# Performance work log

Measured on AMD Instinct MI355X. Metric: run time of the kernel, lower is better.

The kernel has to match this reference:

```python
import jax, jax.numpy as jnp
import numpy as np

N = 50000          # total nodes (types: 20000/17000/13000)
E = 800000         # edges, avg degree 16
NUM_ETYPES = 6
ALPHA = 0.05       # residual-attention blend coefficient
SLOPE = 0.2        # leaky_relu negative slope


def _edge_softmax(e, dst, n):
    # softmax over incoming edges of each destination node; e: [E, H]
    m = jax.ops.segment_max(e, dst, num_segments=n)      # [N, H]
    ex = jnp.exp(e - m[dst])
    s = jax.ops.segment_sum(ex, dst, num_segments=n)     # [N, H]
    return ex / s[dst]


def _gat_layer(h, src, dst, etype, W, We, eemb, al, ar, ae, resW, res_attn, activate):
    n = h.shape[0]
    H, out = al.shape
    feat = (h @ W).reshape(n, H, out)                    # [N, H, out]
    T, edim = eemb.shape
    # edge-type attention term: embedding -> fc_e -> attn_e; only T distinct rows
    et_att = jnp.einsum('thd,hd->th', (eemb @ We).reshape(T, H, edim), ae)  # [T, H]
    el = jnp.einsum('nho,ho->nh', feat, al)              # [N, H]
    er = jnp.einsum('nho,ho->nh', feat, ar)              # [N, H]
    e = jax.nn.leaky_relu(el[src] + er[dst] + et_att[etype], SLOPE)  # [E, H]
    a = _edge_softmax(e, dst, n)                         # [E, H]
    if res_attn is not None:
        a = a * (1.0 - ALPHA) + res_attn * ALPHA
    rst = jax.ops.segment_sum(feat[src] * a[:, :, None], dst, num_segments=n)  # [N, H, out]
    if resW is not None:
        rst = rst + (h @ resW).reshape(n, H, out)
    if activate:
        rst = jax.nn.elu(rst)
    return rst, jax.lax.stop_gradient(a)


def _forward(x0, x1, x2, fcw0, fcb0, fcw1, fcb1, fcw2, fcb2,
             W0, We0, eemb0, al0, ar0, ae0,
             W1, We1, eemb1, al1, ar1, ae1, resW1,
             W2, We2, eemb2, al2, ar2, ae2, resW2,
             src, dst, etype):
    # per-type input projection then concat (feat_drop=0 -> identity)
    h = jnp.concatenate([x0 @ fcw0 + fcb0, x1 @ fcw1 + fcb1, x2 @ fcw2 + fcb2], axis=0)  # [N, 64]
    h1, a = _gat_layer(h, src, dst, etype, W0, We0, eemb0, al0, ar0, ae0, None, None, True)
    h1 = h1.reshape(h1.shape[0], -1)                     # [N, 256]
    h2, a = _gat_layer(h1, src, dst, etype, W1, We1, eemb1, al1, ar1, ae1, resW1, a, True)
    h2 = h2.reshape(h2.shape[0], -1)                     # [N, 256]
    logits, _ = _gat_layer(h2, src, dst, etype, W2, We2, eemb2, al2, ar2, ae2, resW2, None, False)
    return logits                                        # [N, 1, 16]


def setup_inputs():
    key = jax.random.key(0)
    ks = iter(jax.random.split(key, 48))
    def rn(shape, fan_in):
        return jax.random.normal(next(ks), shape, jnp.float32) / np.sqrt(fan_in)
    inp = {}
    inp['x0'] = jax.random.normal(next(ks), (20000, 128), jnp.float32)
    inp['x1'] = jax.random.normal(next(ks), (17000, 256), jnp.float32)
    inp['x2'] = jax.random.normal(next(ks), (13000, 64), jnp.float32)
    inp['fcw0'] = rn((128, 64), 128); inp['fcb0'] = jnp.zeros((64,), jnp.float32)
    inp['fcw1'] = rn((256, 64), 256); inp['fcb1'] = jnp.zeros((64,), jnp.float32)
    inp['fcw2'] = rn((64, 64), 64);   inp['fcb2'] = jnp.zeros((64,), jnp.float32)
    # layer 0: in=64 -> H=8, out=32
    inp['W0'] = rn((64, 256), 64); inp['We0'] = rn((64, 512), 64)
    inp['eemb0'] = rn((NUM_ETYPES, 64), 1.0)
    inp['al0'] = rn((8, 32), 32); inp['ar0'] = rn((8, 32), 32); inp['ae0'] = rn((8, 64), 64)
    # layer 1: in=256 -> H=8, out=32, residual
    inp['W1'] = rn((256, 256), 256); inp['We1'] = rn((64, 512), 64)
    inp['eemb1'] = rn((NUM_ETYPES, 64), 1.0)
    inp['al1'] = rn((8, 32), 32); inp['ar1'] = rn((8, 32), 32); inp['ae1'] = rn((8, 64), 64)
    inp['resW1'] = rn((256, 256), 256)
    # output layer: in=256 -> H=1, out=16, residual
    inp['W2'] = rn((256, 16), 256); inp['We2'] = rn((64, 64), 64)
    inp['eemb2'] = rn((NUM_ETYPES, 64), 1.0)
    inp['al2'] = rn((1, 16), 16); inp['ar2'] = rn((1, 16), 16); inp['ae2'] = rn((1, 64), 64)
    inp['resW2'] = rn((256, 16), 256)
    inp['src'] = jax.random.randint(next(ks), (E,), 0, N)
    inp['dst'] = jax.random.randint(next(ks), (E,), 0, N)
    inp['etype'] = jax.random.randint(next(ks), (E,), 0, NUM_ETYPES)
    return inp


def reference(x0, x1, x2, fcw0, fcb0, fcw1, fcb1, fcw2, fcb2,
              W0, We0, eemb0, al0, ar0, ae0,
              W1, We1, eemb1, al1, ar1, ae1, resW1,
              W2, We2, eemb2, al2, ar2, ae2, resW2,
              src, dst, etype):
    return _forward(x0, x1, x2, fcw0, fcb0, fcw1, fcb1, fcw2, fcb2,
                    W0, We0, eemb0, al0, ar0, ae0,
                    W1, We1, eemb1, al1, ar1, ae1, resW1,
                    W2, We2, eemb2, al2, ar2, ae2, resW2,
                    src, dst, etype)
```

## Files before the change

### kernel.cpp

```cpp
#include <hip/hip_runtime.h>
#include <hip/hip_bf16.h>

#define ALPHA 0.05f
#define SLOPE 0.2f
#define LCAP 128

typedef __attribute__((ext_vector_type(8))) short short8v;
typedef __attribute__((ext_vector_type(8))) unsigned short ushort8v;
typedef __attribute__((ext_vector_type(4))) float floatx4;

__device__ inline ushort f2b(float f) {
    uint u = __float_as_uint(f);
    return (ushort)((u + 0x7fffu + ((u >> 16) & 1u)) >> 16);
}
__device__ inline float b2f(ushort b) { return __uint_as_float(((uint)b) << 16); }

__device__ inline void gload_lds16(const ushort* g, ushort* l) {
    __builtin_amdgcn_global_load_lds(
        (const __attribute__((address_space(1))) uint*)g,
        (__attribute__((address_space(3))) uint*)l, 16, 0, 0);
}


__global__ void hist_kernel(const int* __restrict__ dst, int* __restrict__ counts, int E) {
    int e = blockIdx.x * blockDim.x + threadIdx.x;
    if (e < E) atomicAdd(&counts[dst[e]], 1);
}

__global__ __launch_bounds__(256) void scan_part(const int* __restrict__ counts,
                                                 int* __restrict__ offsets,
                                                 int* __restrict__ partial, int n) {
    __shared__ int sd[256];
    int i = blockIdx.x * 256 + threadIdx.x;
    int v = (i < n) ? counts[i] : 0;
    sd[threadIdx.x] = v;
    __syncthreads();
    for (int off = 1; off < 256; off <<= 1) {
        int t = (threadIdx.x >= off) ? sd[threadIdx.x - off] : 0;
        __syncthreads();
        sd[threadIdx.x] += t;
        __syncthreads();
    }
    if (i < n) offsets[i + 1] = sd[threadIdx.x];
    if (threadIdx.x == 255) partial[blockIdx.x] = sd[255];
}

__global__ __launch_bounds__(256) void scan_top(int* __restrict__ partial, int nb) {
    __shared__ int sd[256];
    int v = (threadIdx.x < nb) ? partial[threadIdx.x] : 0;
    sd[threadIdx.x] = v;
    __syncthreads();
    for (int off = 1; off < 256; off <<= 1) {
        int t = (threadIdx.x >= off) ? sd[threadIdx.x - off] : 0;
        __syncthreads();
        sd[threadIdx.x] += t;
        __syncthreads();
    }
    if (threadIdx.x < nb) partial[threadIdx.x] = sd[threadIdx.x];
}

__global__ __launch_bounds__(256) void scan_add(int* __restrict__ offsets,
                                                int* __restrict__ cursor,
                                                const int* __restrict__ partial, int n) {
    int i = blockIdx.x * 256 + threadIdx.x;
    if (i >= n) return;
    int add = (blockIdx.x > 0) ? partial[blockIdx.x - 1] : 0;
    int v = offsets[i + 1] + add;
    offsets[i + 1] = v;
    if (i + 1 < n) cursor[i + 1] = v;
    if (i == 0) { offsets[0] = 0; cursor[0] = 0; }
}

__global__ void scatter_kernel(const int* __restrict__ src, const int* __restrict__ dst,
                               const int* __restrict__ et, int* __restrict__ cursor,
                               int* __restrict__ se, int E) {
    int e = blockIdx.x * blockDim.x + threadIdx.x;
    if (e >= E) return;
    int d = dst[e];
    int pos = atomicAdd(&cursor[d], 1);
    se[pos] = (src[e] << 3) | et[e];
}


__global__ void wprep3(const float* __restrict__ W0f, const float* __restrict__ W1f,
                       const float* __restrict__ WRf, ushort* __restrict__ Wt0,
                       ushort* __restrict__ Wt1, ushort* __restrict__ WtR) {
    int i = blockIdx.x * blockDim.x + threadIdx.x;
    if (i < 16384) {
        int k = i / 256, n = i % 256;
        Wt0[n * 64 + k] = f2b(W0f[i]);
    } else if (i < 16384 + 65536) {
        int j = i - 16384;
        int k = j / 256, n = j % 256;
        Wt1[n * 256 + k] = f2b(W1f[j]);
    } else if (i < 16384 + 2 * 65536) {
        int j = i - 16384 - 65536;
        int k = j / 256, n = j % 256;
        WtR[n * 256 + k] = f2b(WRf[j]);
    }
}


template<bool ATTN>
__global__ __launch_bounds__(256) void gemm_bf16(const ushort* __restrict__ A,
                                                 const ushort* __restrict__ Bt,
                                                 ushort* __restrict__ Cb,
                                                 const float* __restrict__ al,
                                                 const float* __restrict__ ar,
                                                 float* __restrict__ el,
                                                 float* __restrict__ er,
                                                 int M, int N, int K) {
    __shared__ ushort As[128 * 32];
    __shared__ ushort Bs[128 * 32];
    int bm = blockIdx.y * 128, bn = blockIdx.x * 128;
    int tid = threadIdx.x;
    int wave = tid >> 6, lane = tid & 63;
    int wm = (wave >> 1) * 64, wn = (wave & 1) * 64;
    int r = tid >> 2, c = (tid & 3) * 8;
    floatx4 acc[4][4] = {};
    for (int k0 = 0; k0 < K; k0 += 32) {
        gload_lds16(&A[(long)(bm + r) * K + k0 + c],       &As[(size_t)tid * 8]);
        gload_lds16(&A[(long)(bm + 64 + r) * K + k0 + c],  &As[(size_t)(256 + tid) * 8]);
        gload_lds16(&Bt[(long)(bn + r) * K + k0 + c],      &Bs[(size_t)tid * 8]);
        gload_lds16(&Bt[(long)(bn + 64 + r) * K + k0 + c], &Bs[(size_t)(256 + tid) * 8]);
        __syncthreads();
        int lr = lane & 15, lk = (lane >> 4) * 8;
        short8v af[4], bfr[4];
#pragma unroll
        for (int i = 0; i < 4; ++i)
            af[i] = *reinterpret_cast<const short8v*>(&As[(wm + i * 16 + lr) * 32 + lk]);
#pragma unroll
        for (int j = 0; j < 4; ++j)
            bfr[j] = *reinterpret_cast<const short8v*>(&Bs[(wn + j * 16 + lr) * 32 + lk]);
#pragma unroll
        for (int i = 0; i < 4; ++i)
#pragma unroll
            for (int j = 0; j < 4; ++j)
                acc[i][j] = __builtin_amdgcn_mfma_f32_16x16x32_bf16(af[i], bfr[j], acc[i][j], 0, 0, 0);
        __syncthreads();
    }
    int col = lane & 15, rbase = (lane >> 4) * 4;
#pragma unroll
    for (int i = 0; i < 4; ++i) {
#pragma unroll
        for (int rr = 0; rr < 4; ++rr) {
            int gm = bm + wm + i * 16 + rbase + rr;
            if (gm >= M) continue;
#pragma unroll
            for (int j = 0; j < 4; ++j) {
                int gn = bn + wn + j * 16 + col;
                Cb[(long)gm * N + gn] = f2b(acc[i][j][rr]);
            }
        }
    }
    if (ATTN) {
        int hA = (bn + wn) >> 5;
        float alv[4], arv[4];
#pragma unroll
        for (int j = 0; j < 4; ++j) {
            int h = hA + (j >> 1);
            int o = (j & 1) * 16 + col;
            alv[j] = al[h * 32 + o];
            arv[j] = ar[h * 32 + o];
        }
#pragma unroll
        for (int i = 0; i < 4; ++i) {
#pragma unroll
            for (int rr = 0; rr < 4; ++rr) {
                float slA = acc[i][0][rr] * alv[0] + acc[i][1][rr] * alv[1];
                float slB = acc[i][2][rr] * alv[2] + acc[i][3][rr] * alv[3];
                float srA = acc[i][0][rr] * arv[0] + acc[i][1][rr] * arv[1];
                float srB = acc[i][2][rr] * arv[2] + acc[i][3][rr] * arv[3];
#pragma unroll
                for (int off = 1; off < 16; off <<= 1) {
                    slA += __shfl_xor(slA, off, 64);
                    slB += __shfl_xor(slB, off, 64);
                    srA += __shfl_xor(srA, off, 64);
                    srB += __shfl_xor(srB, off, 64);
                }
                int gm = bm + wm + i * 16 + rbase + rr;
                if (col == 0 && gm < M) {
                    el[gm * 8 + hA]     = slA;
                    el[gm * 8 + hA + 1] = slB;
                    er[gm * 8 + hA]     = srA;
                    er[gm * 8 + hA + 1] = srB;
                }
            }
        }
    }
}


__global__ __launch_bounds__(256) void matmul64_fc3(
    const float* __restrict__ A0, const float* __restrict__ A1, const float* __restrict__ A2,
    const float* __restrict__ W0, const float* __restrict__ W1, const float* __restrict__ W2,
    const float* __restrict__ b0, const float* __restrict__ b1, const float* __restrict__ b2,
    ushort* __restrict__ C, int n0, int n1, int n2) {
    int z = blockIdx.z;
    const float *A, *W, *bias;
    int M, K;
    long coff;
    if (z == 0)      { A = A0; W = W0; bias = b0; M = n0; K = 128; coff = 0; }
    else if (z == 1) { A = A1; W = W1; bias = b1; M = n1; K = 256; coff = (long)n0 * 64; }
    else             { A = A2; W = W2; bias = b2; M = n2; K = 64;  coff = (long)(n0 + n1) * 64; }
    int bm = blockIdx.y * 64;
    if (bm >= M) return;
    __shared__ float As[16][68];
    __shared__ float Bs[16][68];
    int tx = threadIdx.x % 16, ty = threadIdx.x / 16;
    float acc[4][4] = {};
    for (int k0 = 0; k0 < K; k0 += 16) {
        for (int i = threadIdx.x; i < 64 * 16; i += 256) {
            int mm = i / 16, kk = i % 16;
            int gm = bm + mm;
            As[kk][mm] = (gm < M) ? A[(long)gm * K + k0 + kk] : 0.f;
        }
        for (int i = threadIdx.x; i < 16 * 64; i += 256) {
            int kk = i / 64, nn = i % 64;
            Bs[kk][nn] = W[(long)(k0 + kk) * 64 + nn];
        }
        __syncthreads();
#pragma unroll
        for (int kk = 0; kk < 16; ++kk) {
            float a[4], b[4];
#pragma unroll
            for (int i = 0; i < 4; ++i) a[i] = As[kk][ty * 4 + i];
#pragma unroll
            for (int j = 0; j < 4; ++j) b[j] = Bs[kk][tx * 4 + j];
#pragma unroll
            for (int i = 0; i < 4; ++i)
#pragma unroll
                for (int j = 0; j < 4; ++j) acc[i][j] += a[i] * b[j];
        }
        __syncthreads();
    }
#pragma unroll
    for (int i = 0; i < 4; ++i) {
        int gm = bm + ty * 4 + i;
        if (gm >= M) continue;
#pragma unroll
        for (int j = 0; j < 4; ++j) {
            int gn = tx * 4 + j;
            C[coff + (long)gm * 64 + gn] = f2b(acc[i][j] + bias[gn]);
        }
    }
}


template<bool ACC, bool BF16OUT, bool ATTN>
__global__ __launch_bounds__(256) void matmul_n16b(const ushort* __restrict__ A,
                                                   const float* __restrict__ W,
                                                   float* __restrict__ Cf,
                                                   ushort* __restrict__ Cb,
                                                   const float* __restrict__ al,
                                                   const float* __restrict__ ar,
                                                   float* __restrict__ el,
                                                   float* __restrict__ er, int M, int K) {
    __shared__ float Ws[256 * 16];
    for (int i = threadIdx.x; i < K * 16; i += 256) Ws[i] = W[i];
    __syncthreads();
    int m = blockIdx.x * 16 + threadIdx.x / 16;
    int nn = threadIdx.x % 16;
    if (m >= M) return;
    float s = 0.f;
    for (int k8 = 0; k8 < K / 8; ++k8) {
        uint4 v = *reinterpret_cast<const uint4*>(&A[(long)m * K + k8 * 8]);
        const uint* vp = reinterpret_cast<const uint*>(&v);
#pragma unroll
        for (int q = 0; q < 4; ++q) {
            uint w2 = vp[q];
            float f0 = __uint_as_float((w2 & 0xffffu) << 16);
            float f1 = __uint_as_float(w2 & 0xffff0000u);
            int k = k8 * 8 + q * 2;
            s += f0 * Ws[(k + 0) * 16 + nn] + f1 * Ws[(k + 1) * 16 + nn];
        }
    }
    if (BF16OUT) {
        Cb[(long)m * 16 + nn] = f2b(s);
    } else {
        if (ACC) s += Cf[(long)m * 16 + nn];
        Cf[(long)m * 16 + nn] = s;
    }
    if (ATTN) {
        float sl = s * al[nn], sr = s * ar[nn];
#pragma unroll
        for (int off = 1; off < 16; off <<= 1) {
            sl += __shfl_xor(sl, off, 64);
            sr += __shfl_xor(sr, off, 64);
        }
        if (nn == 0) { el[m] = sl; er[m] = sr; }
    }
}


template<int H>
__global__ __launch_bounds__(H * 64) void etype_att(const float* __restrict__ eemb,
                                                    const float* __restrict__ We,
                                                    const float* __restrict__ ae,
                                                    float* __restrict__ out) {
    __shared__ float es[64];
    int t = blockIdx.x;
    int j = threadIdx.x;
    if (j < 64) es[j] = eemb[t * 64 + j];
    __syncthreads();
    float wsum = 0.f;
#pragma unroll 8
    for (int k = 0; k < 64; ++k) wsum += es[k] * We[k * (H * 64) + j];
    float v = wsum * ae[j];
#pragma unroll
    for (int off = 32; off > 0; off >>= 1) v += __shfl_down(v, off, 64);
    if ((j & 63) == 0) out[t * H + (j >> 6)] = v;
}


template<bool BLEND, bool SAVE, bool RES>
__global__ __launch_bounds__(64) void fused_edge_h8(
    const int* __restrict__ offsets, const int* __restrict__ se,
    const float* __restrict__ el, const float* __restrict__ er,
    const float* __restrict__ etatt,
    const ushort* __restrict__ featb,
    const ushort* __restrict__ a0_in, ushort* __restrict__ a0_out,
    const ushort* __restrict__ resin, ushort* __restrict__ outb, int N) {
    int d = blockIdx.x;
    int lane = threadIdx.x;
    int lo = offsets[d], hi = offsets[d + 1];
    int deg = hi - lo;
    __shared__ float a_lds[LCAP][8];
    __shared__ int   s_lds[LCAP];
    __shared__ float er_s[8];
    __shared__ float m_s[8], inv_s[8];
    if (lane < 8) er_s[lane] = er[d * 8 + lane];
    __syncthreads();
    bool fast = (deg <= LCAP);
    if (fast) {
        for (int i = lane; i < deg * 8; i += 64) {
            int p = i >> 3, h = i & 7;
            int v0 = se[lo + p];
            int s = v0 >> 3, t = v0 & 7;
            if (h == 0) s_lds[p] = s;
            float v = el[s * 8 + h] + er_s[h] + etatt[t * 8 + h];
            a_lds[p][h] = v > 0.f ? v : SLOPE * v;
        }
        __syncthreads();
        {
            int g = lane >> 3, h = lane & 7;
            float m = -INFINITY;
            for (int p = g; p < deg; p += 8) m = fmaxf(m, a_lds[p][h]);
#pragma unroll
            for (int off = 8; off < 64; off <<= 1) m = fmaxf(m, __shfl_xor(m, off, 64));
            float ssum = 0.f;
            for (int p = g; p < deg; p += 8) ssum += __expf(a_lds[p][h] - m);
#pragma unroll
            for (int off = 8; off < 64; off <<= 1) ssum += __shfl_xor(ssum, off, 64);
            if (g == 0) {
                m_s[h] = m;
                inv_s[h] = ssum > 0.f ? 1.f / ssum : 0.f;
            }
        }
        __syncthreads();
        for (int i = lane; i < deg * 8; i += 64) {
            int p = i >> 3, h = i & 7;
            float a = __expf(a_lds[p][h] - m_s[h]) * inv_s[h];
            if (BLEND) a = a * (1.f - ALPHA) + b2f(a0_in[lo * 8 + i]) * ALPHA;
            a_lds[p][h] = a;
            if (SAVE) a0_out[lo * 8 + i] = f2b(a);
        }
        __syncthreads();
    } else {
        int g = lane >> 3, h = lane & 7;
        float m = -INFINITY;
        for (int p = g; p < deg; p += 8) {
            int v0 = se[lo + p];
            int s = v0 >> 3, t = v0 & 7;
            float v = el[s * 8 + h] + er_s[h] + etatt[t * 8 + h];
            v = v > 0.f ? v : SLOPE * v;
            m = fmaxf(m, v);
        }
#pragma unroll
        for (int off = 8; off < 64; off <<= 1) m = fmaxf(m, __shfl_xor(m, off, 64));
        float ssum = 0.f;
        for (int p = g; p < deg; p += 8) {
            int v0 = se[lo + p];
            int s = v0 >> 3, t = v0 & 7;
            float v = el[s * 8 + h] + er_s[h] + etatt[t * 8 + h];
            v = v > 0.f ? v : SLOPE * v;
            ssum += __expf(v - m);
        }
#pragma unroll
        for (int off = 8; off < 64; off <<= 1) ssum += __shfl_xor(ssum, off, 64);
        if (g == 0) {
            m_s[h] = m;
            inv_s[h] = ssum > 0.f ? 1.f / ssum : 0.f;
        }
        __syncthreads();
        if (SAVE) {
            for (int i = lane; i < deg * 8; i += 64) {
                int p = i >> 3, hh = i & 7;
                int v0 = se[lo + p];
                int s = v0 >> 3, t = v0 & 7;
                float v = el[s * 8 + hh] + er_s[hh] + etatt[t * 8 + hh];
                v = v > 0.f ? v : SLOPE * v;
                float a = __expf(v - m_s[hh]) * inv_s[hh];
                if (BLEND) a = a * (1.f - ALPHA) + b2f(a0_in[lo * 8 + i]) * ALPHA;
                a0_out[lo * 8 + i] = f2b(a);
            }
        }
    }
    int half = lane >> 5, t = lane & 31;
    float acc[8];
#pragma unroll
    for (int k = 0; k < 8; ++k) acc[k] = 0.f;
    if (RES && half == 0) {
        uint4 rv = *reinterpret_cast<const uint4*>(&resin[(long)d * 256 + t * 8]);
        const uint* rp = reinterpret_cast<const uint*>(&rv);
#pragma unroll
        for (int q = 0; q < 4; ++q) {
            acc[2 * q]     = __uint_as_float(rp[q] << 16);
            acc[2 * q + 1] = __uint_as_float(rp[q] & 0xffff0000u);
        }
    }
    int h = t >> 2;
    if (fast) {
        int p = half;
        for (; p + 6 < deg; p += 8) {
            int s0 = s_lds[p],     s1 = s_lds[p + 2];
            int s2 = s_lds[p + 4], s3 = s_lds[p + 6];
            float a0 = a_lds[p][h],     a1 = a_lds[p + 2][h];
            float a2 = a_lds[p + 4][h], a3 = a_lds[p + 6][h];
            uint4 f0 = *reinterpret_cast<const uint4*>(&featb[(long)s0 * 256 + t * 8]);
            uint4 f1 = *reinterpret_cast<const uint4*>(&featb[(long)s1 * 256 + t * 8]);
            uint4 f2 = *reinterpret_cast<const uint4*>(&featb[(long)s2 * 256 + t * 8]);
            uint4 f3 = *reinterpret_cast<const uint4*>(&featb[(long)s3 * 256 + t * 8]);
            const uint* q0 = reinterpret_cast<const uint*>(&f0);
            const uint* q1 = reinterpret_cast<const uint*>(&f1);
            const uint* q2 = reinterpret_cast<const uint*>(&f2);
            const uint* q3 = reinterpret_cast<const uint*>(&f3);
#pragma unroll
            for (int q = 0; q < 4; ++q) {
                acc[2 * q] += __uint_as_float(q0[q] << 16) * a0
                            + __uint_as_float(q1[q] << 16) * a1
                            + __uint_as_float(q2[q] << 16) * a2
                            + __uint_as_float(q3[q] << 16) * a3;
                acc[2 * q + 1] += __uint_as_float(q0[q] & 0xffff0000u) * a0
                                + __uint_as_float(q1[q] & 0xffff0000u) * a1
                                + __uint_as_float(q2[q] & 0xffff0000u) * a2
                                + __uint_as_float(q3[q] & 0xffff0000u) * a3;
            }
        }
        for (; p < deg; p += 2) {
            int s = s_lds[p];
            float a = a_lds[p][h];
            uint4 fv = *reinterpret_cast<const uint4*>(&featb[(long)s * 256 + t * 8]);
            const uint* fp = reinterpret_cast<const uint*>(&fv);
#pragma unroll
            for (int q = 0; q < 4; ++q) {
                uint u = fp[q];
                acc[2 * q]     += __uint_as_float(u << 16) * a;
                acc[2 * q + 1] += __uint_as_float(u & 0xffff0000u) * a;
            }
        }
    } else {
        for (int p = half; p < deg; p += 2) {
            int v0 = se[lo + p];
            int s = v0 >> 3, tt = v0 & 7;
            float v = el[s * 8 + h] + er_s[h] + etatt[tt * 8 + h];
            v = v > 0.f ? v : SLOPE * v;
            float a = __expf(v - m_s[h]) * inv_s[h];
            if (BLEND) a = a * (1.f - ALPHA) + b2f(a0_in[(long)(lo + p) * 8 + h]) * ALPHA;
            uint4 fv = *reinterpret_cast<const uint4*>(&featb[(long)s * 256 + t * 8]);
            const uint* fp = reinterpret_cast<const uint*>(&fv);
#pragma unroll
            for (int q = 0; q < 4; ++q) {
                uint u = fp[q];
                acc[2 * q]     += __uint_as_float(u << 16) * a;
                acc[2 * q + 1] += __uint_as_float(u & 0xffff0000u) * a;
            }
        }
    }
#pragma unroll
    for (int k = 0; k < 8; ++k) acc[k] += __shfl_down(acc[k], 32);
    if (half == 0) {
        ushort8v o;
#pragma unroll
        for (int k = 0; k < 8; ++k) {
            float v = acc[k];
            v = v > 0.f ? v : __expf(v) - 1.f;
            o[k] = f2b(v);
        }
        *reinterpret_cast<ushort8v*>(&outb[(long)d * 256 + t * 8]) = o;
    }
}


__global__ __launch_bounds__(64) void fused_edge_h1(
    const int* __restrict__ offsets, const int* __restrict__ se,
    const float* __restrict__ el, const float* __restrict__ er,
    const float* __restrict__ etatt,
    const ushort* __restrict__ featb2, float* __restrict__ out, int N) {
    int d = blockIdx.x;
    int lane = threadIdx.x;
    int lo = offsets[d], hi = offsets[d + 1];
    int deg = hi - lo;
    __shared__ float a_lds[512];
    float er_d = er[d];
    bool fast = (deg <= 512);
    float m = -INFINITY, inv = 0.f;
    if (fast) {
        for (int i = lane; i < deg; i += 64) {
            int v0 = se[lo + i];
            int s = v0 >> 3, t = v0 & 7;
            float v = el[s] + er_d + etatt[t];
            a_lds[i] = v > 0.f ? v : SLOPE * v;
        }
        __syncthreads();
        for (int i = lane; i < deg; i += 64) m = fmaxf(m, a_lds[i]);
#pragma unroll
        for (int off = 1; off < 64; off <<= 1) m = fmaxf(m, __shfl_xor(m, off, 64));
        float ssum = 0.f;
        for (int i = lane; i < deg; i += 64) ssum += __expf(a_lds[i] - m);
#pragma unroll
        for (int off = 1; off < 64; off <<= 1) ssum += __shfl_xor(ssum, off, 64);
        inv = ssum > 0.f ? 1.f / ssum : 0.f;
        for (int i = lane; i < deg; i += 64) a_lds[i] = __expf(a_lds[i] - m) * inv;
        __syncthreads();
    } else {
        for (int i = lane; i < deg; i += 64) {
            int v0 = se[lo + i];
            int s = v0 >> 3, t = v0 & 7;
            float v = el[s] + er_d + etatt[t];
            v = v > 0.f ? v : SLOPE * v;
            m = fmaxf(m, v);
        }
#pragma unroll
        for (int off = 1; off < 64; off <<= 1) m = fmaxf(m, __shfl_xor(m, off, 64));
        float ssum = 0.f;
        for (int i = lane; i < deg; i += 64) {
            int v0 = se[lo + i];
            int s = v0 >> 3, t = v0 & 7;
            float v = el[s] + er_d + etatt[t];
            v = v > 0.f ? v : SLOPE * v;
            ssum += __expf(v - m);
        }
#pragma unroll
        for (int off = 1; off < 64; off <<= 1) ssum += __shfl_xor(ssum, off, 64);
        inv = ssum > 0.f ? 1.f / ssum : 0.f;
    }
    int g = lane >> 1, t = lane & 1;
    float acc[8];
#pragma unroll
    for (int k = 0; k < 8; ++k) acc[k] = 0.f;
    for (int p = g; p < deg; p += 32) {
        int v0 = se[lo + p];
        int s = v0 >> 3;
        float a;
        if (fast) a = a_lds[p];
        else {
            int tt = v0 & 7;
            float v = el[s] + er_d + etatt[tt];
            v = v > 0.f ? v : SLOPE * v;
            a = __expf(v - m) * inv;
        }
        uint4 fv = *reinterpret_cast<const uint4*>(&featb2[(long)s * 16 + t * 8]);
        const uint* fp = reinterpret_cast<const uint*>(&fv);
#pragma unroll
        for (int q = 0; q < 4; ++q) {
            acc[2 * q]     += __uint_as_float(fp[q] << 16) * a;
            acc[2 * q + 1] += __uint_as_float(fp[q] & 0xffff0000u) * a;
        }
    }
#pragma unroll
    for (int off = 2; off < 64; off <<= 1)
#pragma unroll
        for (int k = 0; k < 8; ++k) acc[k] += __shfl_down(acc[k], off);
    if (lane < 2) {
        float* op = &out[(long)d * 16 + t * 8];
        *reinterpret_cast<float4*>(op)     = make_float4(acc[0], acc[1], acc[2], acc[3]);
        *reinterpret_cast<float4*>(op + 4) = make_float4(acc[4], acc[5], acc[6], acc[7]);
    }
}


extern "C" void kernel_launch(void* const* d_in, const int* in_sizes, int n_in,
                              void* d_out, int out_size, void* d_ws, size_t ws_size,
                              hipStream_t stream) {
    const float* x0   = (const float*)d_in[0];
    const float* x1   = (const float*)d_in[1];
    const float* x2   = (const float*)d_in[2];
    const float* fcw0 = (const float*)d_in[3];
    const float* fcb0 = (const float*)d_in[4];
    const float* fcw1 = (const float*)d_in[5];
    const float* fcb1 = (const float*)d_in[6];
    const float* fcw2 = (const float*)d_in[7];
    const float* fcb2 = (const float*)d_in[8];
    const float* W0   = (const float*)d_in[9];
    const float* We0  = (const float*)d_in[10];
    const float* eemb0= (const float*)d_in[11];
    const float* al0  = (const float*)d_in[12];
    const float* ar0  = (const float*)d_in[13];
    const float* ae0  = (const float*)d_in[14];
    const float* W1   = (const float*)d_in[15];
    const float* We1  = (const float*)d_in[16];
    const float* eemb1= (const float*)d_in[17];
    const float* al1  = (const float*)d_in[18];
    const float* ar1  = (const float*)d_in[19];
    const float* ae1  = (const float*)d_in[20];
    const float* resW1= (const float*)d_in[21];
    const float* W2   = (const float*)d_in[22];
    const float* We2  = (const float*)d_in[23];
    const float* eemb2= (const float*)d_in[24];
    const float* al2  = (const float*)d_in[25];
    const float* ar2  = (const float*)d_in[26];
    const float* ae2  = (const float*)d_in[27];
    const float* resW2= (const float*)d_in[28];
    const int* src    = (const int*)d_in[29];
    const int* dst    = (const int*)d_in[30];
    const int* etype  = (const int*)d_in[31];

    const int n0 = in_sizes[0] / 128;
    const int n1 = in_sizes[1] / 256;
    const int n2 = in_sizes[2] / 64;
    const int N  = n0 + n1 + n2;
    const int E  = in_sizes[29];

    char* w = (char*)d_ws;
    auto alloc = [&](size_t bytes) {
        char* p = w;
        w += (bytes + 255) & ~(size_t)255;
        return p;
    };
    int*    counts  = (int*)alloc((size_t)N * 4);
    int*    offsets = (int*)alloc((size_t)(N + 1) * 4);
    int*    cursor  = (int*)alloc((size_t)N * 4);
    int*    partial = (int*)alloc(1024 * 4);
    int*    se      = (int*)alloc((size_t)E * 4);
    ushort* h2res   = (ushort*)alloc((size_t)N * 256 * 2);
    ushort* a0b     = (ushort*)alloc((size_t)E * 8 * 2);
    ushort* h0bf    = (ushort*)alloc((size_t)N * 64 * 2 + 128 * 256 * 2);
    ushort* featb   = (ushort*)alloc((size_t)N * 256 * 2);
    ushort* h1bf    = (ushort*)alloc((size_t)N * 256 * 2 + 128 * 256 * 2);
    ushort* h2bf    = (ushort*)alloc((size_t)N * 256 * 2);
    float*  el      = (float*)alloc((size_t)N * 8 * 4);
    float*  er      = (float*)alloc((size_t)N * 8 * 4);
    float*  etatt   = (float*)alloc(6 * 8 * 4);
    ushort* Wt0     = (ushort*)alloc((size_t)256 * 64 * 2);
    ushort* Wt1     = (ushort*)alloc((size_t)256 * 256 * 2);
    ushort* WtR     = (ushort*)alloc((size_t)256 * 256 * 2);
    ushort* feat2b  = (ushort*)alloc((size_t)N * 16 * 2);
    float*  out     = (float*)d_out;

    const int TB = 256;
    int eb = (E + TB - 1) / TB;
    int nb1 = (N + 255) / 256;

    hipMemsetAsync(counts, 0, (size_t)N * 4, stream);
    hist_kernel<<<eb, TB, 0, stream>>>(dst, counts, E);
    scan_part<<<nb1, 256, 0, stream>>>(counts, offsets, partial, N);
    scan_top<<<1, 256, 0, stream>>>(partial, nb1);
    scan_add<<<nb1, 256, 0, stream>>>(offsets, cursor, partial, N);
    scatter_kernel<<<eb, TB, 0, stream>>>(src, dst, etype, cursor, se, E);

    wprep3<<<(16384 + 2 * 65536 + TB - 1) / TB, TB, 0, stream>>>(W0, W1, resW1, Wt0, Wt1, WtR);

    {
        int maxTiles = (n0 + 63) / 64;
        int t1 = (n1 + 63) / 64, t2 = (n2 + 63) / 64;
        if (t1 > maxTiles) maxTiles = t1;
        if (t2 > maxTiles) maxTiles = t2;
        dim3 g(1, maxTiles, 3);
        matmul64_fc3<<<g, TB, 0, stream>>>(x0, x1, x2, fcw0, fcw1, fcw2,
                                           fcb0, fcb1, fcb2, h0bf, n0, n1, n2);
    }

    dim3 gg(256 / 128, (N + 127) / 128);

    {
        gemm_bf16<true><<<gg, TB, 0, stream>>>(h0bf, Wt0, featb, al0, ar0, el, er, N, 256, 64);
        etype_att<8><<<6, 512, 0, stream>>>(eemb0, We0, ae0, etatt);
        fused_edge_h8<false, true, false><<<N, 64, 0, stream>>>(
            offsets, se, el, er, etatt, featb, nullptr, a0b, nullptr, h1bf, N);
    }

    {
        gemm_bf16<true><<<gg, TB, 0, stream>>>(h1bf, Wt1, featb, al1, ar1, el, er, N, 256, 256);
        etype_att<8><<<6, 512, 0, stream>>>(eemb1, We1, ae1, etatt);
        gemm_bf16<false><<<gg, TB, 0, stream>>>(h1bf, WtR, h2res, nullptr, nullptr, nullptr, nullptr, N, 256, 256);
        fused_edge_h8<true, false, true><<<N, 64, 0, stream>>>(
            offsets, se, el, er, etatt, featb, a0b, nullptr, h2res, h2bf, N);
    }

    {
        matmul_n16b<false, true, true><<<(N + 15) / 16, TB, 0, stream>>>(
            h2bf, W2, nullptr, feat2b, al2, ar2, el, er, N, 256);
        etype_att<1><<<6, 64, 0, stream>>>(eemb2, We2, ae2, etatt);
        fused_edge_h1<<<N, 64, 0, stream>>>(offsets, se, el, er, etatt, feat2b, out, N);
        matmul_n16b<true, false, false><<<(N + 15) / 16, TB, 0, stream>>>(
            h2bf, resW2, out, nullptr, nullptr, nullptr, nullptr, nullptr, N, 256);
    }
}
```

Baseline: 450.9 us.

## Fuse dual GEMMs, batch etype attention, prefetch features in edge aggregation

```diff
diff --git a/kernel.cpp b/kernel.cpp
--- a/kernel.cpp
+++ b/kernel.cpp
@@ -98,6 +98,32 @@
         int k = j / 256, n = j % 256;
         WtR[n * 256 + k] = f2b(WRf[j]);
     }
+}
+
+
+__global__ __launch_bounds__(512) void etype_all(
+    const float* __restrict__ eemb0, const float* __restrict__ We0, const float* __restrict__ ae0, float* __restrict__ out0,
+    const float* __restrict__ eemb1, const float* __restrict__ We1, const float* __restrict__ ae1, float* __restrict__ out1,
+    const float* __restrict__ eemb2, const float* __restrict__ We2, const float* __restrict__ ae2, float* __restrict__ out2) {
+    int layer = blockIdx.x / 6, t = blockIdx.x % 6;
+    const float *eemb, *We, *ae;
+    float* out;
+    int H;
+    if (layer == 0)      { eemb = eemb0; We = We0; ae = ae0; out = out0; H = 8; }
+    else if (layer == 1) { eemb = eemb1; We = We1; ae = ae1; out = out1; H = 8; }
+    else                 { eemb = eemb2; We = We2; ae = ae2; out = out2; H = 1; }
+    __shared__ float es[64];
+    int j = threadIdx.x;
+    if (j < 64) es[j] = eemb[t * 64 + j];
+    __syncthreads();
+    if (j >= H * 64) return;
+    float wsum = 0.f;
+#pragma unroll 8
+    for (int k = 0; k < 64; ++k) wsum += es[k] * We[k * (H * 64) + j];
+    float v = wsum * ae[j];
+#pragma unroll
+    for (int off = 32; off > 0; off >>= 1) v += __shfl_down(v, off, 64);
+    if ((j & 63) == 0) out[t * H + (j >> 6)] = v;
 }
 
 
@@ -185,6 +211,108 @@
                     er[gm * 8 + hA]     = srA;
                     er[gm * 8 + hA + 1] = srB;
                 }
+            }
+        }
+    }
+}
+
+
+__global__ __launch_bounds__(256) void gemm_dual(const ushort* __restrict__ A,
+                                                 const ushort* __restrict__ B1,
+                                                 const ushort* __restrict__ B2,
+                                                 ushort* __restrict__ C1,
+                                                 ushort* __restrict__ C2,
+                                                 const float* __restrict__ al,
+                                                 const float* __restrict__ ar,
+                                                 float* __restrict__ el,
+                                                 float* __restrict__ er,
+                                                 int M, int N, int K) {
+    __shared__ ushort As[128 * 32];
+    __shared__ ushort Bs1[128 * 32];
+    __shared__ ushort Bs2[128 * 32];
+    int bm = blockIdx.y * 128, bn = blockIdx.x * 128;
+    int tid = threadIdx.x;
+    int wave = tid >> 6, lane = tid & 63;
+    int wm = (wave >> 1) * 64, wn = (wave & 1) * 64;
+    int r = tid >> 2, c = (tid & 3) * 8;
+    floatx4 acc1[4][4] = {};
+    floatx4 acc2[4][4] = {};
+    for (int k0 = 0; k0 < K; k0 += 32) {
+        gload_lds16(&A[(long)(bm + r) * K + k0 + c],        &As[(size_t)tid * 8]);
+        gload_lds16(&A[(long)(bm + 64 + r) * K + k0 + c],   &As[(size_t)(256 + tid) * 8]);
+        gload_lds16(&B1[(long)(bn + r) * K + k0 + c],       &Bs1[(size_t)tid * 8]);
+        gload_lds16(&B1[(long)(bn + 64 + r) * K + k0 + c],  &Bs1[(size_t)(256 + tid) * 8]);
+        gload_lds16(&B2[(long)(bn + r) * K + k0 + c],       &Bs2[(size_t)tid * 8]);
+        gload_lds16(&B2[(long)(bn + 64 + r) * K + k0 + c],  &Bs2[(size_t)(256 + tid) * 8]);
+        __syncthreads();
+        int lr = lane & 15, lk = (lane >> 4) * 8;
+        short8v af[4], bfr[4];
+#pragma unroll
+        for (int i = 0; i < 4; ++i)
+            af[i] = *reinterpret_cast<const short8v*>(&As[(wm + i * 16 + lr) * 32 + lk]);
+#pragma unroll
+        for (int j = 0; j < 4; ++j)
+            bfr[j] = *reinterpret_cast<const short8v*>(&Bs1[(wn + j * 16 + lr) * 32 + lk]);
+#pragma unroll
+        for (int i = 0; i < 4; ++i)
+#pragma unroll
+            for (int j = 0; j < 4; ++j)
+                acc1[i][j] = __builtin_amdgcn_mfma_f32_16x16x32_bf16(af[i], bfr[j], acc1[i][j], 0, 0, 0);
+#pragma unroll
+        for (int j = 0; j < 4; ++j)
+            bfr[j] = *reinterpret_cast<const short8v*>(&Bs2[(wn + j * 16 + lr) * 32 + lk]);
+#pragma unroll
+        for (int i = 0; i < 4; ++i)
+#pragma unroll
+            for (int j = 0; j < 4; ++j)
+                acc2[i][j] = __builtin_amdgcn_mfma_f32_16x16x32_bf16(af[i], bfr[j], acc2[i][j], 0, 0, 0);
+        __syncthreads();
+    }
+    int col = lane & 15, rbase = (lane >> 4) * 4;
+#pragma unroll
+    for (int i = 0; i < 4; ++i) {
+#pragma unroll
+        for (int rr = 0; rr < 4; ++rr) {
+            int gm = bm + wm + i * 16 + rbase + rr;
+            if (gm >= M) continue;
+#pragma unroll
+            for (int j = 0; j < 4; ++j) {
+                int gn = bn + wn + j * 16 + col;
+                C1[(long)gm * N + gn] = f2b(acc1[i][j][rr]);
+                C2[(long)gm * N + gn] = f2b(acc2[i][j][rr]);
+            }
+        }
+    }
+    int hA = (bn + wn) >> 5;
+    float alv[4], arv[4];
+#pragma unroll
+    for (int j = 0; j < 4; ++j) {
+        int h = hA + (j >> 1);
+        int o = (j & 1) * 16 + col;
+        alv[j] = al[h * 32 + o];
+        arv[j] = ar[h * 32 + o];
+    }
+#pragma unroll
+    for (int i = 0; i < 4; ++i) {
+#pragma unroll
+        for (int rr = 0; rr < 4; ++rr) {
+            float slA = acc1[i][0][rr] * alv[0] + acc1[i][1][rr] * alv[1];
+            float slB = acc1[i][2][rr] * alv[2] + acc1[i][3][rr] * alv[3];
+            float srA = acc1[i][0][rr] * arv[0] + acc1[i][1][rr] * arv[1];
+            float srB = acc1[i][2][rr] * arv[2] + acc1[i][3][rr] * arv[3];
+#pragma unroll
+            for (int off = 1; off < 16; off <<= 1) {
+                slA += __shfl_xor(slA, off, 64);
+                slB += __shfl_xor(slB, off, 64);
+                srA += __shfl_xor(srA, off, 64);
+                srB += __shfl_xor(srB, off, 64);
+            }
+            int gm = bm + wm + i * 16 + rbase + rr;
+            if (col == 0 && gm < M) {
+                el[gm * 8 + hA]     = slA;
+                el[gm * 8 + hA + 1] = slB;
+                er[gm * 8 + hA]     = srA;
+                er[gm * 8 + hA + 1] = srB;
             }
         }
     }
@@ -247,42 +375,45 @@
 }
 
 
-template<bool ACC, bool BF16OUT, bool ATTN>
-__global__ __launch_bounds__(256) void matmul_n16b(const ushort* __restrict__ A,
-                                                   const float* __restrict__ W,
-                                                   float* __restrict__ Cf,
-                                                   ushort* __restrict__ Cb,
-                                                   const float* __restrict__ al,
-                                                   const float* __restrict__ ar,
-                                                   float* __restrict__ el,
-                                                   float* __restrict__ er, int M, int K) {
-    __shared__ float Ws[256 * 16];
-    for (int i = threadIdx.x; i < K * 16; i += 256) Ws[i] = W[i];
+__global__ __launch_bounds__(256) void matmul_n16_dual(const ushort* __restrict__ A,
+                                                       const float* __restrict__ W2,
+                                                       const float* __restrict__ WR,
+                                                       ushort* __restrict__ feat2b,
+                                                       float* __restrict__ resout,
+                                                       const float* __restrict__ al,
+                                                       const float* __restrict__ ar,
+                                                       float* __restrict__ el,
+                                                       float* __restrict__ er, int M) {
+    __shared__ float Ws2[256 * 16];
+    __shared__ float WsR[256 * 16];
+    for (int i = threadIdx.x; i < 256 * 16; i += 256) {
+        Ws2[i] = W2[i];
+        WsR[i] = WR[i];
+    }
     __syncthreads();
-    int m = blockIdx.x * 16 + threadIdx.x / 16;
     int nn = threadIdx.x % 16;
-    if (m >= M) return;
-    float s = 0.f;
-    for (int k8 = 0; k8 < K / 8; ++k8) {
-        uint4 v = *reinterpret_cast<const uint4*>(&A[(long)m * K + k8 * 8]);
-        const uint* vp = reinterpret_cast<const uint*>(&v);
-#pragma unroll
-        for (int q = 0; q < 4; ++q) {
-            uint w2 = vp[q];
-            float f0 = __uint_as_float((w2 & 0xffffu) << 16);
-            float f1 = __uint_as_float(w2 & 0xffff0000u);
-            int k = k8 * 8 + q * 2;
-            s += f0 * Ws[(k + 0) * 16 + nn] + f1 * Ws[(k + 1) * 16 + nn];
-        }
-    }
-    if (BF16OUT) {
-        Cb[(long)m * 16 + nn] = f2b(s);
-    } else {
-        if (ACC) s += Cf[(long)m * 16 + nn];
-        Cf[(long)m * 16 + nn] = s;
-    }
-    if (ATTN) {
-        float sl = s * al[nn], sr = s * ar[nn];
+    float alv = al[nn], arv = ar[nn];
+#pragma unroll
+    for (int rb = 0; rb < 2; ++rb) {
+        int m = blockIdx.x * 32 + rb * 16 + threadIdx.x / 16;
+        if (m >= M) continue;
+        float s1 = 0.f, s2 = 0.f;
+        for (int k8 = 0; k8 < 32; ++k8) {
+            uint4 v = *reinterpret_cast<const uint4*>(&A[(long)m * 256 + k8 * 8]);
+            const uint* vp = reinterpret_cast<const uint*>(&v);
+#pragma unroll
+            for (int q = 0; q < 4; ++q) {
+                uint w2 = vp[q];
+                float f0 = __uint_as_float((w2 & 0xffffu) << 16);
+                float f1 = __uint_as_float(w2 & 0xffff0000u);
+                int k = k8 * 8 + q * 2;
+                s1 += f0 * Ws2[(k + 0) * 16 + nn] + f1 * Ws2[(k + 1) * 16 + nn];
+                s2 += f0 * WsR[(k + 0) * 16 + nn] + f1 * WsR[(k + 1) * 16 + nn];
+            }
+        }
+        feat2b[(long)m * 16 + nn] = f2b(s1);
+        resout[(long)m * 16 + nn] = s2;
+        float sl = s1 * alv, sr = s1 * arv;
 #pragma unroll
         for (int off = 1; off < 16; off <<= 1) {
             sl += __shfl_xor(sl, off, 64);
@@ -290,26 +421,6 @@
         }
         if (nn == 0) { el[m] = sl; er[m] = sr; }
     }
-}
-
-
-template<int H>
-__global__ __launch_bounds__(H * 64) void etype_att(const float* __restrict__ eemb,
-                                                    const float* __restrict__ We,
-                                                    const float* __restrict__ ae,
-                                                    float* __restrict__ out) {
-    __shared__ float es[64];
-    int t = blockIdx.x;
-    int j = threadIdx.x;
-    if (j < 64) es[j] = eemb[t * 64 + j];
-    __syncthreads();
-    float wsum = 0.f;
-#pragma unroll 8
-    for (int k = 0; k < 64; ++k) wsum += es[k] * We[k * (H * 64) + j];
-    float v = wsum * ae[j];
-#pragma unroll
-    for (int off = 32; off > 0; off >>= 1) v += __shfl_down(v, off, 64);
-    if ((j & 63) == 0) out[t * H + (j >> 6)] = v;
 }
 
 
@@ -332,16 +443,28 @@
     if (lane < 8) er_s[lane] = er[d * 8 + lane];
     __syncthreads();
     bool fast = (deg <= LCAP);
+    int half = lane >> 5, t = lane & 31;
+    int h8 = t >> 2;
+    uint4 pf[4];
+    int npf = 0;
     if (fast) {
         for (int i = lane; i < deg * 8; i += 64) {
             int p = i >> 3, h = i & 7;
             int v0 = se[lo + p];
-            int s = v0 >> 3, t = v0 & 7;
+            int s = v0 >> 3, tt = v0 & 7;
             if (h == 0) s_lds[p] = s;
-            float v = el[s * 8 + h] + er_s[h] + etatt[t * 8 + h];
+            float v = el[s * 8 + h] + er_s[h] + etatt[tt * 8 + h];
             a_lds[p][h] = v > 0.f ? v : SLOPE * v;
         }
         __syncthreads();
+#pragma unroll
+        for (int u = 0; u < 4; ++u) {
+            int p = half + 2 * u;
+            if (p < deg) {
+                pf[u] = *reinterpret_cast<const uint4*>(&featb[(long)s_lds[p] * 256 + t * 8]);
+                npf = u + 1;
+            }
+        }
         {
             int g = lane >> 3, h = lane & 7;
             float m = -INFINITY;
@@ -371,8 +494,8 @@
         float m = -INFINITY;
         for (int p = g; p < deg; p += 8) {
             int v0 = se[lo + p];
-            int s = v0 >> 3, t = v0 & 7;
-            float v = el[s * 8 + h] + er_s[h] + etatt[t * 8 + h];
+            int s = v0 >> 3, tt = v0 & 7;
+            float v = el[s * 8 + h] + er_s[h] + etatt[tt * 8 + h];
             v = v > 0.f ? v : SLOPE * v;
             m = fmaxf(m, v);
         }
@@ -381,8 +504,8 @@
         float ssum = 0.f;
         for (int p = g; p < deg; p += 8) {
             int v0 = se[lo + p];
-            int s = v0 >> 3, t = v0 & 7;
-            float v = el[s * 8 + h] + er_s[h] + etatt[t * 8 + h];
+            int s = v0 >> 3, tt = v0 & 7;
+            float v = el[s * 8 + h] + er_s[h] + etatt[tt * 8 + h];
             v = v > 0.f ? v : SLOPE * v;
             ssum += __expf(v - m);
         }
@@ -397,8 +520,8 @@
             for (int i = lane; i < deg * 8; i += 64) {
                 int p = i >> 3, hh = i & 7;
                 int v0 = se[lo + p];
-                int s = v0 >> 3, t = v0 & 7;
-                float v = el[s * 8 + hh] + er_s[hh] + etatt[t * 8 + hh];
+                int s = v0 >> 3, tt = v0 & 7;
+                float v = el[s * 8 + hh] + er_s[hh] + etatt[tt * 8 + hh];
                 v = v > 0.f ? v : SLOPE * v;
                 float a = __expf(v - m_s[hh]) * inv_s[hh];
                 if (BLEND) a = a * (1.f - ALPHA) + b2f(a0_in[lo * 8 + i]) * ALPHA;
@@ -406,7 +529,6 @@
             }
         }
     }
-    int half = lane >> 5, t = lane & 31;
     float acc[8];
 #pragma unroll
     for (int k = 0; k < 8; ++k) acc[k] = 0.f;
@@ -419,14 +541,25 @@
             acc[2 * q + 1] = __uint_as_float(rp[q] & 0xffff0000u);
         }
     }
-    int h = t >> 2;
     if (fast) {
-        int p = half;
+#pragma unroll
+        for (int u = 0; u < 4; ++u) {
+            if (u < npf) {
+                float a = a_lds[half + 2 * u][h8];
+                const uint* fp = reinterpret_cast<const uint*>(&pf[u]);
+#pragma unroll
+                for (int q = 0; q < 4; ++q) {
+                    acc[2 * q]     += __uint_as_float(fp[q] << 16) * a;
+                    acc[2 * q + 1] += __uint_as_float(fp[q] & 0xffff0000u) * a;
+                }
+            }
+        }
+        int p = half + 8;
         for (; p + 6 < deg; p += 8) {
             int s0 = s_lds[p],     s1 = s_lds[p + 2];
             int s2 = s_lds[p + 4], s3 = s_lds[p + 6];
-            float a0 = a_lds[p][h],     a1 = a_lds[p + 2][h];
-            float a2 = a_lds[p + 4][h], a3 = a_lds[p + 6][h];
+            float a0 = a_lds[p][h8],     a1 = a_lds[p + 2][h8];
+            float a2 = a_lds[p + 4][h8], a3 = a_lds[p + 6][h8];
             uint4 f0 = *reinterpret_cast<const uint4*>(&featb[(long)s0 * 256 + t * 8]);
             uint4 f1 = *reinterpret_cast<const uint4*>(&featb[(long)s1 * 256 + t * 8]);
             uint4 f2 = *reinterpret_cast<const uint4*>(&featb[(long)s2 * 256 + t * 8]);
@@ -449,7 +582,7 @@
         }
         for (; p < deg; p += 2) {
             int s = s_lds[p];
-            float a = a_lds[p][h];
+            float a = a_lds[p][h8];
             uint4 fv = *reinterpret_cast<const uint4*>(&featb[(long)s * 256 + t * 8]);
             const uint* fp = reinterpret_cast<const uint*>(&fv);
 #pragma unroll
@@ -463,10 +596,10 @@
         for (int p = half; p < deg; p += 2) {
             int v0 = se[lo + p];
             int s = v0 >> 3, tt = v0 & 7;
-            float v = el[s * 8 + h] + er_s[h] + etatt[tt * 8 + h];
+            float v = el[s * 8 + h8] + er_s[h8] + etatt[tt * 8 + h8];
             v = v > 0.f ? v : SLOPE * v;
-            float a = __expf(v - m_s[h]) * inv_s[h];
-            if (BLEND) a = a * (1.f - ALPHA) + b2f(a0_in[(long)(lo + p) * 8 + h]) * ALPHA;
+            float a = __expf(v - m_s[h8]) * inv_s[h8];
+            if (BLEND) a = a * (1.f - ALPHA) + b2f(a0_in[(long)(lo + p) * 8 + h8]) * ALPHA;
             uint4 fv = *reinterpret_cast<const uint4*>(&featb[(long)s * 256 + t * 8]);
             const uint* fp = reinterpret_cast<const uint*>(&fv);
 #pragma unroll
@@ -496,7 +629,8 @@
     const int* __restrict__ offsets, const int* __restrict__ se,
     const float* __restrict__ el, const float* __restrict__ er,
     const float* __restrict__ etatt,
-    const ushort* __restrict__ featb2, float* __restrict__ out, int N) {
+    const ushort* __restrict__ featb2, const float* __restrict__ resout,
+    float* __restrict__ out, int N) {
     int d = blockIdx.x;
     int lane = threadIdx.x;
     int lo = offsets[d], hi = offsets[d + 1];
@@ -573,9 +707,12 @@
 #pragma unroll
         for (int k = 0; k < 8; ++k) acc[k] += __shfl_down(acc[k], off);
     if (lane < 2) {
+        const float* rp = &resout[(long)d * 16 + t * 8];
+        float4 r0 = *reinterpret_cast<const float4*>(rp);
+        float4 r1 = *reinterpret_cast<const float4*>(rp + 4);
         float* op = &out[(long)d * 16 + t * 8];
-        *reinterpret_cast<float4*>(op)     = make_float4(acc[0], acc[1], acc[2], acc[3]);
-        *reinterpret_cast<float4*>(op + 4) = make_float4(acc[4], acc[5], acc[6], acc[7]);
+        *reinterpret_cast<float4*>(op)     = make_float4(acc[0] + r0.x, acc[1] + r0.y, acc[2] + r0.z, acc[3] + r0.w);
+        *reinterpret_cast<float4*>(op + 4) = make_float4(acc[4] + r1.x, acc[5] + r1.y, acc[6] + r1.z, acc[7] + r1.w);
     }
 }
 
@@ -641,11 +778,14 @@
     ushort* h2bf    = (ushort*)alloc((size_t)N * 256 * 2);
     float*  el      = (float*)alloc((size_t)N * 8 * 4);
     float*  er      = (float*)alloc((size_t)N * 8 * 4);
-    float*  etatt   = (float*)alloc(6 * 8 * 4);
+    float*  etatt0  = (float*)alloc(64 * 4);
+    float*  etatt1  = (float*)alloc(64 * 4);
+    float*  etatt2  = (float*)alloc(64 * 4);
     ushort* Wt0     = (ushort*)alloc((size_t)256 * 64 * 2);
     ushort* Wt1     = (ushort*)alloc((size_t)256 * 256 * 2);
     ushort* WtR     = (ushort*)alloc((size_t)256 * 256 * 2);
     ushort* feat2b  = (ushort*)alloc((size_t)N * 16 * 2);
+    float*  resout  = (float*)alloc((size_t)N * 16 * 4);
     float*  out     = (float*)d_out;
 
     const int TB = 256;
@@ -660,6 +800,9 @@
     scatter_kernel<<<eb, TB, 0, stream>>>(src, dst, etype, cursor, se, E);
 
     wprep3<<<(16384 + 2 * 65536 + TB - 1) / TB, TB, 0, stream>>>(W0, W1, resW1, Wt0, Wt1, WtR);
+    etype_all<<<18, 512, 0, stream>>>(eemb0, We0, ae0, etatt0,
+                                      eemb1, We1, ae1, etatt1,
+                                      eemb2, We2, ae2, etatt2);
 
     {
         int maxTiles = (n0 + 63) / 64;
@@ -673,27 +816,15 @@
 
     dim3 gg(256 / 128, (N + 127) / 128);
 
-    {
-        gemm_bf16<true><<<gg, TB, 0, stream>>>(h0bf, Wt0, featb, al0, ar0, el, er, N, 256, 64);
-        etype_att<8><<<6, 512, 0, stream>>>(eemb0, We0, ae0, etatt);
-        fused_edge_h8<false, true, false><<<N, 64, 0, stream>>>(
-            offsets, se, el, er, etatt, featb, nullptr, a0b, nullptr, h1bf, N);
-    }
-
-    {
-        gemm_bf16<true><<<gg, TB, 0, stream>>>(h1bf, Wt1, featb, al1, ar1, el, er, N, 256, 256);
-        etype_att<8><<<6, 512, 0, stream>>>(eemb1, We1, ae1, etatt);
-        gemm_bf16<false><<<gg, TB, 0, stream>>>(h1bf, WtR, h2res, nullptr, nullptr, nullptr, nullptr, N, 256, 256);
-        fused_edge_h8<true, false, true><<<N, 64, 0, stream>>>(
-            offsets, se, el, er, etatt, featb, a0b, nullptr, h2res, h2bf, N);
-    }
-
-    {
-        matmul_n16b<false, true, true><<<(N + 15) / 16, TB, 0, stream>>>(
-            h2bf, W2, nullptr, feat2b, al2, ar2, el, er, N, 256);
-        etype_att<1><<<6, 64, 0, stream>>>(eemb2, We2, ae2, etatt);
-        fused_edge_h1<<<N, 64, 0, stream>>>(offsets, se, el, er, etatt, feat2b, out, N);
-        matmul_n16b<true, false, false><<<(N + 15) / 16, TB, 0, stream>>>(
-            h2bf, resW2, out, nullptr, nullptr, nullptr, nullptr, nullptr, N, 256);
-    }
-}
+    gemm_bf16<true><<<gg, TB, 0, stream>>>(h0bf, Wt0, featb, al0, ar0, el, er, N, 256, 64);
+    fused_edge_h8<false, true, false><<<N, 64, 0, stream>>>(
+        offsets, se, el, er, etatt0, featb, nullptr, a0b, nullptr, h1bf, N);
+
+    gemm_dual<<<gg, TB, 0, stream>>>(h1bf, Wt1, WtR, featb, h2res, al1, ar1, el, er, N, 256, 256);
+    fused_edge_h8<true, false, true><<<N, 64, 0, stream>>>(
+        offsets, se, el, er, etatt1, featb, a0b, nullptr, h2res, h2bf, N);
+
+    matmul_n16_dual<<<(N + 31) / 32, TB, 0, stream>>>(
+        h2bf, W2, resW2, feat2b, resout, al2, ar2, el, er, N);
+    fused_edge_h1<<<N, 64, 0, stream>>>(offsets, se, el, er, etatt2, feat2b, resout, out, N);
+}
```

Result: faster. 441.6 us (-2.1%).
